# Performance work log

Measured on AMD Instinct MI355X. Metric: run time of the kernel, lower is better.

Reference implementation:

```python
import jax, jax.numpy as jnp
import numpy as np


def setup_inputs() -> dict:
    key = jax.random.key(0)
    kx, ky = jax.random.split(key)
    x = jax.random.normal(kx, (16, 4096, 3), dtype=jnp.float32)
    y = jax.random.normal(ky, (16, 4096, 3), dtype=jnp.float32)
    return {"x": x, "y": y}


def reference(x, y):
    # avoiding the O(b*N*M*d) difference tensor of the naive expansion.
    x2 = jnp.sum(x * x, axis=-1)                  # (b, N)
    y2 = jnp.sum(y * y, axis=-1)                  # (b, M)
    xy = jnp.einsum('bnd,bmd->bnm', x, y)         # (b, N, M)
    dist = x2[:, :, None] + y2[:, None, :] - 2.0 * xy
    min_d = jnp.min(dist, axis=2)                 # top-1 smallest over M -> (b, N)
    chamfer = jnp.sum(min_d, axis=1) / x.shape[1] # (b,)
    return jnp.sum(chamfer)
```

## Files before the change

kernel.cpp:

```cpp
#include <hip/hip_runtime.h>


constexpr int NPTS   = 4096;
constexpr int NBATCH = 16;
constexpr int BLOCK  = 256;


constexpr int XPT16 = 16;
constexpr int NYC64 = 64;
constexpr int YT64  = NPTS / NYC64;

__global__ __launch_bounds__(BLOCK, 4) void chamfer_part16_kernel(
    const float* __restrict__ x, const float* __restrict__ y,
    float* __restrict__ ws)
{
    __shared__ float4 sy[YT64];

    const int b      = blockIdx.x / NYC64;
    const int ychunk = blockIdx.x % NYC64;

    if (threadIdx.x < YT64) {
        const float* yp = y + ((size_t)b * NPTS + ychunk * YT64 + threadIdx.x) * 3;
        const float y0 = yp[0], y1 = yp[1], y2 = yp[2];
        sy[threadIdx.x] = make_float4(2.0f * y0, 2.0f * y1, 2.0f * y2,
                                      fmaf(y2, y2, fmaf(y1, y1, y0 * y0)));
    }

    const int xbase = threadIdx.x * XPT16;
    const float4* xp4 = (const float4*)(x + ((size_t)b * NPTS + xbase) * 3);
    float xf[48];
    #pragma unroll
    for (int q = 0; q < 12; ++q) {
        const float4 a = xp4[q];
        xf[4 * q + 0] = a.x; xf[4 * q + 1] = a.y;
        xf[4 * q + 2] = a.z; xf[4 * q + 3] = a.w;
    }

    __syncthreads();

    float m[XPT16];
    #pragma unroll
    for (int i = 0; i < XPT16; ++i) m[i] = 3.4e38f;

    #pragma unroll 2
    for (int j = 0; j < YT64; j += 2) {
        const float4 Y0 = sy[j];
        const float4 Y1 = sy[j + 1];
        #pragma unroll
        for (int i = 0; i < XPT16; ++i) {
            const float t0 = fmaf(-xf[3 * i + 0], Y0.x,
                             fmaf(-xf[3 * i + 1], Y0.y,
                             fmaf(-xf[3 * i + 2], Y0.z, Y0.w)));
            const float t1 = fmaf(-xf[3 * i + 0], Y1.x,
                             fmaf(-xf[3 * i + 1], Y1.y,
                             fmaf(-xf[3 * i + 2], Y1.z, Y1.w)));
            m[i] = fminf(fminf(t0, t1), m[i]);
        }
    }

    float* wp = ws + ((size_t)b * NYC64 + ychunk) * NPTS + xbase;
    #pragma unroll
    for (int i = 0; i < XPT16; i += 4) {
        float4 o;
        float* oc = (float*)&o;
        #pragma unroll
        for (int k = 0; k < 4; ++k) {
            const int p = i + k;
            const float x2 = fmaf(xf[3 * p + 2], xf[3 * p + 2],
                             fmaf(xf[3 * p + 1], xf[3 * p + 1],
                                  xf[3 * p + 0] * xf[3 * p + 0]));
            oc[k] = fmaxf(x2 + m[p], 0.0f);
        }
        ((float4*)wp)[i / 4] = o;
    }
}

__global__ __launch_bounds__(BLOCK) void chamfer_reduce64_kernel(
    const float* __restrict__ ws, float* __restrict__ out)
{
    __shared__ float swsum[BLOCK / 64];
    const int idx = blockIdx.x * BLOCK + threadIdx.x;
    const int b   = idx / NPTS;
    const int xp  = idx % NPTS;

    const float* p = ws + (size_t)b * NYC64 * NPTS + xp;
    float mn = 3.4e38f;
    #pragma unroll 8
    for (int yc = 0; yc < NYC64; ++yc)
        mn = fminf(mn, p[(size_t)yc * NPTS]);

    float s = mn;
    for (int off = 32; off > 0; off >>= 1)
        s += __shfl_down(s, off, 64);
    const int wave = threadIdx.x >> 6;
    if ((threadIdx.x & 63) == 0) swsum[wave] = s;
    __syncthreads();
    if (threadIdx.x == 0) {
        float t = 0.f;
        #pragma unroll
        for (int w = 0; w < BLOCK / 64; ++w) t += swsum[w];
        atomicAdd(out, t * (1.0f / NPTS));
    }
}


constexpr int XPT    = 8;
constexpr int XCHUNK = BLOCK * XPT;
constexpr int NXC    = NPTS / XCHUNK;

template <int NYC>
__global__ __launch_bounds__(BLOCK, 4) void chamfer_part_kernel(
    const float* __restrict__ x, const float* __restrict__ y,
    float* __restrict__ ws)
{
    constexpr int YTILE = NPTS / NYC;
    __shared__ float4 sy[YTILE];

    const int b      = blockIdx.x / (NXC * NYC);
    const int xchunk = (blockIdx.x / NYC) % NXC;
    const int ychunk = blockIdx.x % NYC;

    for (int i = threadIdx.x; i < YTILE; i += BLOCK) {
        const float* yp = y + ((size_t)b * NPTS + ychunk * YTILE + i) * 3;
        const float y0 = yp[0], y1 = yp[1], y2 = yp[2];
        sy[i] = make_float4(2.0f * y0, 2.0f * y1, 2.0f * y2,
                            fmaf(y2, y2, fmaf(y1, y1, y0 * y0)));
    }

    const int xbase = xchunk * XCHUNK + threadIdx.x * XPT;
    const float4* xp4 = (const float4*)(x + ((size_t)b * NPTS + xbase) * 3);
    const float4 a0 = xp4[0], a1 = xp4[1], a2 = xp4[2];
    const float4 a3 = xp4[3], a4 = xp4[4], a5 = xp4[5];
    const float xa[XPT][3] = {
        {a0.x, a0.y, a0.z}, {a0.w, a1.x, a1.y},
        {a1.z, a1.w, a2.x}, {a2.y, a2.z, a2.w},
        {a3.x, a3.y, a3.z}, {a3.w, a4.x, a4.y},
        {a4.z, a4.w, a5.x}, {a5.y, a5.z, a5.w}};

    float x2s[XPT];
    #pragma unroll
    for (int i = 0; i < XPT; ++i)
        x2s[i] = fmaf(xa[i][2], xa[i][2],
                 fmaf(xa[i][1], xa[i][1], xa[i][0] * xa[i][0]));

    __syncthreads();

    float m[XPT];
    #pragma unroll
    for (int i = 0; i < XPT; ++i) m[i] = 3.4e38f;

    #pragma unroll 2
    for (int j = 0; j < YTILE; j += 2) {
        const float4 Y0 = sy[j];
        const float4 Y1 = sy[j + 1];
        #pragma unroll
        for (int i = 0; i < XPT; ++i) {
            const float t0 = fmaf(-xa[i][0], Y0.x,
                             fmaf(-xa[i][1], Y0.y,
                             fmaf(-xa[i][2], Y0.z, Y0.w)));
            const float t1 = fmaf(-xa[i][0], Y1.x,
                             fmaf(-xa[i][1], Y1.y,
                             fmaf(-xa[i][2], Y1.z, Y1.w)));
            m[i] = fminf(fminf(t0, t1), m[i]);
        }
    }

    float* wp = ws + ((size_t)b * NYC + ychunk) * NPTS + xbase;
    #pragma unroll
    for (int i = 0; i < XPT; i += 4) {
        float4 o;
        float* oc = (float*)&o;
        #pragma unroll
        for (int k = 0; k < 4; ++k)
            oc[k] = fmaxf(x2s[i + k] + m[i + k], 0.0f);
        ((float4*)wp)[i / 4] = o;
    }
}

template <int NYC>
__global__ __launch_bounds__(BLOCK) void chamfer_reduce_kernel(
    const float* __restrict__ ws, float* __restrict__ out)
{
    __shared__ float swsum[BLOCK / 64];
    const int idx = blockIdx.x * BLOCK + threadIdx.x;
    const int b   = idx / NPTS;
    const int xp  = idx % NPTS;

    float mn = 3.4e38f;
    #pragma unroll
    for (int yc = 0; yc < NYC; ++yc)
        mn = fminf(mn, ws[((size_t)b * NYC + yc) * NPTS + xp]);

    float s = mn;
    for (int off = 32; off > 0; off >>= 1)
        s += __shfl_down(s, off, 64);
    const int wave = threadIdx.x >> 6;
    if ((threadIdx.x & 63) == 0) swsum[wave] = s;
    __syncthreads();
    if (threadIdx.x == 0) {
        float t = 0.f;
        #pragma unroll
        for (int w = 0; w < BLOCK / 64; ++w) t += swsum[w];
        atomicAdd(out, t * (1.0f / NPTS));
    }
}


__global__ __launch_bounds__(BLOCK) void chamfer_min_atomic_kernel(
    const float* __restrict__ x, const float* __restrict__ y,
    unsigned int* __restrict__ ws_min)
{
    constexpr int YTILE = 256;
    constexpr int NYC   = NPTS / YTILE;
    __shared__ float4 sy[YTILE];

    const int b      = blockIdx.x / (NXC * NYC);
    const int xchunk = (blockIdx.x / NYC) % NXC;
    const int ychunk = blockIdx.x % NYC;

    {
        const float* yp = y + ((size_t)b * NPTS + ychunk * YTILE + threadIdx.x) * 3;
        const float y0 = yp[0], y1 = yp[1], y2 = yp[2];
        sy[threadIdx.x] = make_float4(2.0f * y0, 2.0f * y1, 2.0f * y2,
                                      fmaf(y2, y2, fmaf(y1, y1, y0 * y0)));
    }

    const int xbase = xchunk * XCHUNK + threadIdx.x * XPT;
    const float4* xp4 = (const float4*)(x + ((size_t)b * NPTS + xbase) * 3);
    const float4 a0 = xp4[0], a1 = xp4[1], a2 = xp4[2];
    const float4 a3 = xp4[3], a4 = xp4[4], a5 = xp4[5];
    const float xa[XPT][3] = {
        {a0.x, a0.y, a0.z}, {a0.w, a1.x, a1.y},
        {a1.z, a1.w, a2.x}, {a2.y, a2.z, a2.w},
        {a3.x, a3.y, a3.z}, {a3.w, a4.x, a4.y},
        {a4.z, a4.w, a5.x}, {a5.y, a5.z, a5.w}};

    float x2s[XPT];
    #pragma unroll
    for (int i = 0; i < XPT; ++i)
        x2s[i] = fmaf(xa[i][2], xa[i][2],
                 fmaf(xa[i][1], xa[i][1], xa[i][0] * xa[i][0]));

    __syncthreads();

    float m[XPT];
    #pragma unroll
    for (int i = 0; i < XPT; ++i) m[i] = 3.4e38f;

    #pragma unroll 2
    for (int j = 0; j < YTILE; j += 2) {
        const float4 Y0 = sy[j];
        const float4 Y1 = sy[j + 1];
        #pragma unroll
        for (int i = 0; i < XPT; ++i) {
            const float t0 = fmaf(-xa[i][0], Y0.x,
                             fmaf(-xa[i][1], Y0.y,
                             fmaf(-xa[i][2], Y0.z, Y0.w)));
            const float t1 = fmaf(-xa[i][0], Y1.x,
                             fmaf(-xa[i][1], Y1.y,
                             fmaf(-xa[i][2], Y1.z, Y1.w)));
            m[i] = fminf(m[i], fminf(t0, t1));
        }
    }

    unsigned int* wm = ws_min + (size_t)b * NPTS + xbase;
    #pragma unroll
    for (int i = 0; i < XPT; ++i) {
        const float d = fmaxf(x2s[i] + m[i], 0.0f);
        atomicMin(&wm[i], __float_as_uint(d));
    }
}

__global__ __launch_bounds__(BLOCK) void chamfer_sum_kernel(
    const unsigned int* __restrict__ ws_min, float* __restrict__ out)
{
    __shared__ float swsum[BLOCK / 64];
    const int total = NBATCH * NPTS;
    float s = 0.f;
    for (int i = blockIdx.x * BLOCK + threadIdx.x; i < total;
         i += gridDim.x * BLOCK)
        s += __uint_as_float(ws_min[i]);

    for (int off = 32; off > 0; off >>= 1)
        s += __shfl_down(s, off, 64);
    const int wave = threadIdx.x >> 6;
    if ((threadIdx.x & 63) == 0) swsum[wave] = s;
    __syncthreads();
    if (threadIdx.x == 0) {
        float t = 0.f;
        #pragma unroll
        for (int w = 0; w < BLOCK / 64; ++w) t += swsum[w];
        atomicAdd(out, t * (1.0f / NPTS));
    }
}


extern "C" void kernel_launch(void* const* d_in, const int* in_sizes, int n_in,
                              void* d_out, int out_size, void* d_ws, size_t ws_size,
                              hipStream_t stream) {
    const float* x = (const float*)d_in[0];
    const float* y = (const float*)d_in[1];
    float* out = (float*)d_out;

    hipMemsetAsync(out, 0, sizeof(float), stream);

    const size_t need64 = (size_t)NBATCH * NYC64 * NPTS * sizeof(float);
    const size_t need16 = (size_t)NBATCH * 16 * NPTS * sizeof(float);

    if (ws_size >= need64) {
        float* ws = (float*)d_ws;
        chamfer_part16_kernel<<<NBATCH * NYC64, BLOCK, 0, stream>>>(x, y, ws);
        chamfer_reduce64_kernel<<<NBATCH * NPTS / BLOCK, BLOCK, 0, stream>>>(ws, out);
    } else if (ws_size >= need16) {
        float* ws = (float*)d_ws;
        chamfer_part_kernel<16><<<NBATCH * NXC * 16, BLOCK, 0, stream>>>(x, y, ws);
        chamfer_reduce_kernel<16><<<NBATCH * NPTS / BLOCK, BLOCK, 0, stream>>>(ws, out);
    } else {
        unsigned int* ws_min = (unsigned int*)d_ws;
        hipMemsetAsync(ws_min, 0xFF, (size_t)NBATCH * NPTS * sizeof(unsigned int),
                       stream);
        chamfer_min_atomic_kernel<<<NBATCH * NXC * 16, BLOCK, 0, stream>>>(
            x, y, ws_min);
        chamfer_sum_kernel<<<64, BLOCK, 0, stream>>>(ws_min, out);
    }
}
```

Measured before the change: 95.82 us.

## Pre-pack y into float4 buffer and stream it via uniform scalar loads

Adds a pack kernel that converts y into (2y, |y|^2) float4 records in the workspace. The main distance kernel then reads these records directly from global memory with block-uniform addresses, so the compiler can use scalar (SGPR) loads, and LDS staging and the block barrier go away. The work split changes from 64 y-chunks with 16 x points per thread to 32 y-chunks with 8 x points per thread. This costs an extra kernel launch and relies on scalar loads keeping pace with the FMA loop, while halving the size of the partial-min workspace.

```diff
diff --git a/kernel.cpp b/kernel.cpp
--- a/kernel.cpp
+++ b/kernel.cpp
@@ -4,128 +4,32 @@
 constexpr int NPTS   = 4096;
 constexpr int NBATCH = 16;
 constexpr int BLOCK  = 256;
-
-
-constexpr int XPT16 = 16;
-constexpr int NYC64 = 64;
-constexpr int YT64  = NPTS / NYC64;
-
-__global__ __launch_bounds__(BLOCK, 4) void chamfer_part16_kernel(
-    const float* __restrict__ x, const float* __restrict__ y,
-    float* __restrict__ ws)
-{
-    __shared__ float4 sy[YT64];
-
-    const int b      = blockIdx.x / NYC64;
-    const int ychunk = blockIdx.x % NYC64;
-
-    if (threadIdx.x < YT64) {
-        const float* yp = y + ((size_t)b * NPTS + ychunk * YT64 + threadIdx.x) * 3;
-        const float y0 = yp[0], y1 = yp[1], y2 = yp[2];
-        sy[threadIdx.x] = make_float4(2.0f * y0, 2.0f * y1, 2.0f * y2,
-                                      fmaf(y2, y2, fmaf(y1, y1, y0 * y0)));
-    }
-
-    const int xbase = threadIdx.x * XPT16;
-    const float4* xp4 = (const float4*)(x + ((size_t)b * NPTS + xbase) * 3);
-    float xf[48];
-    #pragma unroll
-    for (int q = 0; q < 12; ++q) {
-        const float4 a = xp4[q];
-        xf[4 * q + 0] = a.x; xf[4 * q + 1] = a.y;
-        xf[4 * q + 2] = a.z; xf[4 * q + 3] = a.w;
-    }
-
-    __syncthreads();
-
-    float m[XPT16];
-    #pragma unroll
-    for (int i = 0; i < XPT16; ++i) m[i] = 3.4e38f;
-
-    #pragma unroll 2
-    for (int j = 0; j < YT64; j += 2) {
-        const float4 Y0 = sy[j];
-        const float4 Y1 = sy[j + 1];
-        #pragma unroll
-        for (int i = 0; i < XPT16; ++i) {
-            const float t0 = fmaf(-xf[3 * i + 0], Y0.x,
-                             fmaf(-xf[3 * i + 1], Y0.y,
-                             fmaf(-xf[3 * i + 2], Y0.z, Y0.w)));
-            const float t1 = fmaf(-xf[3 * i + 0], Y1.x,
-                             fmaf(-xf[3 * i + 1], Y1.y,
-                             fmaf(-xf[3 * i + 2], Y1.z, Y1.w)));
-            m[i] = fminf(fminf(t0, t1), m[i]);
-        }
-    }
-
-    float* wp = ws + ((size_t)b * NYC64 + ychunk) * NPTS + xbase;
-    #pragma unroll
-    for (int i = 0; i < XPT16; i += 4) {
-        float4 o;
-        float* oc = (float*)&o;
-        #pragma unroll
-        for (int k = 0; k < 4; ++k) {
-            const int p = i + k;
-            const float x2 = fmaf(xf[3 * p + 2], xf[3 * p + 2],
-                             fmaf(xf[3 * p + 1], xf[3 * p + 1],
-                                  xf[3 * p + 0] * xf[3 * p + 0]));
-            oc[k] = fmaxf(x2 + m[p], 0.0f);
-        }
-        ((float4*)wp)[i / 4] = o;
-    }
-}
-
-__global__ __launch_bounds__(BLOCK) void chamfer_reduce64_kernel(
-    const float* __restrict__ ws, float* __restrict__ out)
-{
-    __shared__ float swsum[BLOCK / 64];
-    const int idx = blockIdx.x * BLOCK + threadIdx.x;
-    const int b   = idx / NPTS;
-    const int xp  = idx % NPTS;
-
-    const float* p = ws + (size_t)b * NYC64 * NPTS + xp;
-    float mn = 3.4e38f;
-    #pragma unroll 8
-    for (int yc = 0; yc < NYC64; ++yc)
-        mn = fminf(mn, p[(size_t)yc * NPTS]);
-
-    float s = mn;
-    for (int off = 32; off > 0; off >>= 1)
-        s += __shfl_down(s, off, 64);
-    const int wave = threadIdx.x >> 6;
-    if ((threadIdx.x & 63) == 0) swsum[wave] = s;
-    __syncthreads();
-    if (threadIdx.x == 0) {
-        float t = 0.f;
-        #pragma unroll
-        for (int w = 0; w < BLOCK / 64; ++w) t += swsum[w];
-        atomicAdd(out, t * (1.0f / NPTS));
-    }
-}
-
-
 constexpr int XPT    = 8;
 constexpr int XCHUNK = BLOCK * XPT;
 constexpr int NXC    = NPTS / XCHUNK;
 
-template <int NYC>
-__global__ __launch_bounds__(BLOCK, 4) void chamfer_part_kernel(
-    const float* __restrict__ x, const float* __restrict__ y,
+constexpr int NYC32  = 32;
+constexpr int YT32   = NPTS / NYC32;
+
+
+__global__ __launch_bounds__(BLOCK) void chamfer_pack_kernel(
+    const float* __restrict__ y, float4* __restrict__ pws)
+{
+    const int idx = blockIdx.x * BLOCK + threadIdx.x;
+    const float* yp = y + (size_t)idx * 3;
+    const float y0 = yp[0], y1 = yp[1], y2 = yp[2];
+    pws[idx] = make_float4(2.0f * y0, 2.0f * y1, 2.0f * y2,
+                           fmaf(y2, y2, fmaf(y1, y1, y0 * y0)));
+}
+
+
+__global__ __launch_bounds__(BLOCK, 4) void chamfer_part_sgpr_kernel(
+    const float* __restrict__ x, const float4* __restrict__ pws,
     float* __restrict__ ws)
 {
-    constexpr int YTILE = NPTS / NYC;
-    __shared__ float4 sy[YTILE];
-
-    const int b      = blockIdx.x / (NXC * NYC);
-    const int xchunk = (blockIdx.x / NYC) % NXC;
-    const int ychunk = blockIdx.x % NYC;
-
-    for (int i = threadIdx.x; i < YTILE; i += BLOCK) {
-        const float* yp = y + ((size_t)b * NPTS + ychunk * YTILE + i) * 3;
-        const float y0 = yp[0], y1 = yp[1], y2 = yp[2];
-        sy[i] = make_float4(2.0f * y0, 2.0f * y1, 2.0f * y2,
-                            fmaf(y2, y2, fmaf(y1, y1, y0 * y0)));
-    }
+    const int b      = blockIdx.x / (NXC * NYC32);
+    const int xchunk = (blockIdx.x / NYC32) % NXC;
+    const int ychunk = blockIdx.x % NYC32;
 
     const int xbase = xchunk * XCHUNK + threadIdx.x * XPT;
     const float4* xp4 = (const float4*)(x + ((size_t)b * NPTS + xbase) * 3);
@@ -137,6 +41,113 @@
         {a3.x, a3.y, a3.z}, {a3.w, a4.x, a4.y},
         {a4.z, a4.w, a5.x}, {a5.y, a5.z, a5.w}};
 
+    float m[XPT];
+    #pragma unroll
+    for (int i = 0; i < XPT; ++i) m[i] = 3.4e38f;
+
+    const float4* yq = pws + (size_t)b * NPTS + ychunk * YT32;
+
+    auto body = [&](const float4& Ya, const float4& Yb) {
+        const float ynA = Ya.w;
+        const float ynB = Yb.w;
+        #pragma unroll
+        for (int i = 0; i < XPT; ++i) {
+            const float t0 = fmaf(-xa[i][0], Ya.x,
+                             fmaf(-xa[i][1], Ya.y,
+                             fmaf(-xa[i][2], Ya.z, ynA)));
+            const float t1 = fmaf(-xa[i][0], Yb.x,
+                             fmaf(-xa[i][1], Yb.y,
+                             fmaf(-xa[i][2], Yb.z, ynB)));
+            m[i] = fminf(fminf(t0, t1), m[i]);
+        }
+    };
+
+    float4 Ya = yq[0], Yb = yq[1];
+    #pragma unroll 2
+    for (int j = 0; j < YT32 - 2; j += 2) {
+        const float4 Yc = yq[j + 2];
+        const float4 Yd = yq[j + 3];
+        body(Ya, Yb);
+        Ya = Yc; Yb = Yd;
+    }
+    body(Ya, Yb);
+
+    float* wp = ws + ((size_t)b * NYC32 + ychunk) * NPTS + xbase;
+    #pragma unroll
+    for (int i = 0; i < XPT; i += 4) {
+        float4 o;
+        float* oc = (float*)&o;
+        #pragma unroll
+        for (int k = 0; k < 4; ++k) {
+            const int p = i + k;
+            const float x2 = fmaf(xa[p][2], xa[p][2],
+                             fmaf(xa[p][1], xa[p][1],
+                                  xa[p][0] * xa[p][0]));
+            oc[k] = fmaxf(x2 + m[p], 0.0f);
+        }
+        ((float4*)wp)[i / 4] = o;
+    }
+}
+
+
+template <int NYC>
+__global__ __launch_bounds__(BLOCK) void chamfer_reduce_kernel(
+    const float* __restrict__ ws, float* __restrict__ out)
+{
+    __shared__ float swsum[BLOCK / 64];
+    const int idx = blockIdx.x * BLOCK + threadIdx.x;
+    const int b   = idx / NPTS;
+    const int xp  = idx % NPTS;
+
+    float mn = 3.4e38f;
+    #pragma unroll 8
+    for (int yc = 0; yc < NYC; ++yc)
+        mn = fminf(mn, ws[((size_t)b * NYC + yc) * NPTS + xp]);
+
+    float s = mn;
+    for (int off = 32; off > 0; off >>= 1)
+        s += __shfl_down(s, off, 64);
+    const int wave = threadIdx.x >> 6;
+    if ((threadIdx.x & 63) == 0) swsum[wave] = s;
+    __syncthreads();
+    if (threadIdx.x == 0) {
+        float t = 0.f;
+        #pragma unroll
+        for (int w = 0; w < BLOCK / 64; ++w) t += swsum[w];
+        atomicAdd(out, t * (1.0f / NPTS));
+    }
+}
+
+
+template <int NYC>
+__global__ __launch_bounds__(BLOCK, 4) void chamfer_part_lds_kernel(
+    const float* __restrict__ x, const float* __restrict__ y,
+    float* __restrict__ ws)
+{
+    constexpr int YTILE = NPTS / NYC;
+    __shared__ float4 sy[YTILE];
+
+    const int b      = blockIdx.x / (NXC * NYC);
+    const int xchunk = (blockIdx.x / NYC) % NXC;
+    const int ychunk = blockIdx.x % NYC;
+
+    for (int i = threadIdx.x; i < YTILE; i += BLOCK) {
+        const float* yp = y + ((size_t)b * NPTS + ychunk * YTILE + i) * 3;
+        const float y0 = yp[0], y1 = yp[1], y2 = yp[2];
+        sy[i] = make_float4(2.0f * y0, 2.0f * y1, 2.0f * y2,
+                            fmaf(y2, y2, fmaf(y1, y1, y0 * y0)));
+    }
+
+    const int xbase = xchunk * XCHUNK + threadIdx.x * XPT;
+    const float4* xp4 = (const float4*)(x + ((size_t)b * NPTS + xbase) * 3);
+    const float4 a0 = xp4[0], a1 = xp4[1], a2 = xp4[2];
+    const float4 a3 = xp4[3], a4 = xp4[4], a5 = xp4[5];
+    const float xa[XPT][3] = {
+        {a0.x, a0.y, a0.z}, {a0.w, a1.x, a1.y},
+        {a1.z, a1.w, a2.x}, {a2.y, a2.z, a2.w},
+        {a3.x, a3.y, a3.z}, {a3.w, a4.x, a4.y},
+        {a4.z, a4.w, a5.x}, {a5.y, a5.z, a5.w}};
+
     float x2s[XPT];
     #pragma unroll
     for (int i = 0; i < XPT; ++i)
@@ -177,34 +188,6 @@
     }
 }
 
-template <int NYC>
-__global__ __launch_bounds__(BLOCK) void chamfer_reduce_kernel(
-    const float* __restrict__ ws, float* __restrict__ out)
-{
-    __shared__ float swsum[BLOCK / 64];
-    const int idx = blockIdx.x * BLOCK + threadIdx.x;
-    const int b   = idx / NPTS;
-    const int xp  = idx % NPTS;
-
-    float mn = 3.4e38f;
-    #pragma unroll
-    for (int yc = 0; yc < NYC; ++yc)
-        mn = fminf(mn, ws[((size_t)b * NYC + yc) * NPTS + xp]);
-
-    float s = mn;
-    for (int off = 32; off > 0; off >>= 1)
-        s += __shfl_down(s, off, 64);
-    const int wave = threadIdx.x >> 6;
-    if ((threadIdx.x & 63) == 0) swsum[wave] = s;
-    __syncthreads();
-    if (threadIdx.x == 0) {
-        float t = 0.f;
-        #pragma unroll
-        for (int w = 0; w < BLOCK / 64; ++w) t += swsum[w];
-        atomicAdd(out, t * (1.0f / NPTS));
-    }
-}
-
 
 __global__ __launch_bounds__(BLOCK) void chamfer_min_atomic_kernel(
     const float* __restrict__ x, const float* __restrict__ y,
@@ -304,17 +287,25 @@
 
     hipMemsetAsync(out, 0, sizeof(float), stream);
 
-    const size_t need64 = (size_t)NBATCH * NYC64 * NPTS * sizeof(float);
-    const size_t need16 = (size_t)NBATCH * 16 * NPTS * sizeof(float);
-
-    if (ws_size >= need64) {
-        float* ws = (float*)d_ws;
-        chamfer_part16_kernel<<<NBATCH * NYC64, BLOCK, 0, stream>>>(x, y, ws);
-        chamfer_reduce64_kernel<<<NBATCH * NPTS / BLOCK, BLOCK, 0, stream>>>(ws, out);
+    const size_t part_bytes = (size_t)NBATCH * NYC32 * NPTS * sizeof(float);
+    const size_t pack_bytes = (size_t)NBATCH * NPTS * sizeof(float4);
+    const size_t need_main  = part_bytes + pack_bytes;
+    const size_t need16     = (size_t)NBATCH * 16 * NPTS * sizeof(float);
+
+    if (ws_size >= need_main) {
+        float*  ws  = (float*)d_ws;
+        float4* pws = (float4*)((char*)d_ws + part_bytes);
+        chamfer_pack_kernel<<<NBATCH * NPTS / BLOCK, BLOCK, 0, stream>>>(y, pws);
+        chamfer_part_sgpr_kernel<<<NBATCH * NXC * NYC32, BLOCK, 0, stream>>>(
+            x, pws, ws);
+        chamfer_reduce_kernel<NYC32><<<NBATCH * NPTS / BLOCK, BLOCK, 0, stream>>>(
+            ws, out);
     } else if (ws_size >= need16) {
         float* ws = (float*)d_ws;
-        chamfer_part_kernel<16><<<NBATCH * NXC * 16, BLOCK, 0, stream>>>(x, y, ws);
-        chamfer_reduce_kernel<16><<<NBATCH * NPTS / BLOCK, BLOCK, 0, stream>>>(ws, out);
+        chamfer_part_lds_kernel<16><<<NBATCH * NXC * 16, BLOCK, 0, stream>>>(
+            x, y, ws);
+        chamfer_reduce_kernel<16><<<NBATCH * NPTS / BLOCK, BLOCK, 0, stream>>>(
+            ws, out);
     } else {
         unsigned int* ws_min = (unsigned int*)d_ws;
         hipMemsetAsync(ws_min, 0xFF, (size_t)NBATCH * NPTS * sizeof(unsigned int),
```

Result: slower. 101.1 us (+5.5%).
